# Kernel tuning notes

Measured on AMD Instinct MI355X. Metric: run time of the kernel, lower is better.

Reference implementation:

```python
import jax, jax.numpy as jnp
import numpy as np

B, S, H = 32, 8192, 512


def setup_inputs() -> dict:
    key = jax.random.key(0)
    k1, k2, k3, k4 = jax.random.split(key, 4)
    output = jax.random.normal(k1, (B, 1, H), dtype=jnp.float32)
    context = jax.random.normal(k2, (B, S, H), dtype=jnp.float32)
    split_index = jax.random.randint(k3, (B,), 1, S - 1)  # avoid all-masked softmax rows
    W = jax.random.normal(k4, (H, 4 * H), dtype=jnp.float32) * (1.0 / np.sqrt(4 * H))
    b = jnp.zeros((H,), dtype=jnp.float32)
    return {"output": output, "context": context, "split_index": split_index, "W": W, "b": b}


def reference(output, context, split_index, W, b):
    Bb, Ss, Hh = context.shape
    rows = jnp.arange(Bb)
    pos = jnp.arange(Ss)

    # attn = bmm(output, context^T).squeeze(1) -> [B, S]
    attn = jnp.einsum('bih,bsh->bis', output, context)[:, 0, :]
    # torch code uses attn.data (detached) for all softmax paths
    attn_d = jax.lax.stop_gradient(attn)

    # forward-side mask: positions i < split_index kept
    fmask = pos[None, :] < split_index[:, None]  # [B, S] bool
    f_logits = jnp.where(fmask, attn_d, -jnp.inf)
    f_attn = jax.nn.softmax(f_logits, axis=1)
    f_attn = f_attn.at[rows, split_index].set(0.0)  # explicit zero at split position
    a_mix = jnp.einsum('bs,bsh->bh', f_attn, context)[:, None, :]  # [B,1,H]

    # NOTE: original source has `b_attn = f_attn.view(...)` (bug), so b_mix == a_mix.
    # The b-side masked softmax is computed but dead; we replicate the realized math.
    b_mix = a_mix

    # det_att = context[b, split_index[b], :]
    det_att = context[rows, split_index][:, None, :]  # [B,1,H]

    combined = jnp.concatenate((a_mix, b_mix, det_att, output), axis=2)  # [B,1,4H]
    out = jnp.tanh(combined @ W.T + b)  # Linear(4H->H) + Tanh, [B,1,H]
    return out, attn
```

## Files before the change

### kernel.cpp

```cpp
#include <hip/hip_runtime.h>
#include <math.h>

#define BATCH 32
#define SEQ   8192
#define HID   512
#define STRIPES 16
#define RPB   (SEQ / STRIPES)
#define CR    16
#define NCHUNK (RPB / CR)

typedef float f4 __attribute__((ext_vector_type(4)));

#define VMWAIT(N) do { asm volatile("s_waitcnt vmcnt(" #N ")" ::: "memory"); \
                       __builtin_amdgcn_sched_barrier(0); } while (0)
#define LGKMWAIT0 do { asm volatile("s_waitcnt lgkmcnt(0)" ::: "memory"); \
                       __builtin_amdgcn_sched_barrier(0); } while (0)

__device__ __forceinline__ void gload_lds(const float* g, float* l) {
  __builtin_amdgcn_global_load_lds(
      (const __attribute__((address_space(1))) void*)g,
      (__attribute__((address_space(3))) void*)l, 16, 0, 0);
}

__global__ __launch_bounds__(256, 2) void k_pass1(
    const float* __restrict__ outp, const float* __restrict__ ctx,
    const int* __restrict__ split, float* __restrict__ attn_out,
    float* __restrict__ pacc, float* __restrict__ pmd)
{
  __shared__ float lds[2][CR][HID];
  const int tid = threadIdx.x, lane = tid & 63, wave = tid >> 6;
  const int b = blockIdx.x >> 4;
  const int stripe = blockIdx.x & 15;
  const int sp = split[b];
  const int s_base = stripe * RPB;

  const float* ob = outp + b * HID + lane * 8;
  const f4 o0 = *(const f4*)ob;
  const f4 o1 = *(const f4*)(ob + 4);

  const float* cbase = ctx + ((size_t)b * SEQ + s_base) * HID;
  float* ao = attn_out + (size_t)b * SEQ + s_base;

#pragma unroll
  for (int i = 0; i < 8; ++i) {
    const int o = (wave * 8 + i) * 256;
    gload_lds(cbase + o + lane * 4, &lds[0][0][0] + o);
  }
#pragma unroll
  for (int i = 0; i < 8; ++i) {
    const int o = (wave * 8 + i) * 256;
    gload_lds(cbase + CR * HID + o + lane * 4, &lds[1][0][0] + o);
  }

  float m = -INFINITY, d = 0.f;
  f4 acc0 = {0.f, 0.f, 0.f, 0.f}, acc1 = {0.f, 0.f, 0.f, 0.f};

#pragma unroll 1
  for (int c = 0; c < NCHUNK; ++c) {
    if (c == 0)                 VMWAIT(8);
    else if (c == NCHUNK - 1)   VMWAIT(1);
    else                        VMWAIT(9);

    const int cur = c & 1;
    f4 c0[4], c1[4];
#pragma unroll
    for (int k = 0; k < 4; ++k) {
      const float* rp = &lds[cur][wave * 4 + k][lane * 8];
      c0[k] = *(const f4*)rp;
      c1[k] = *(const f4*)(rp + 4);
    }
    LGKMWAIT0;

    if (c + 2 < NCHUNK) {
      const float* src = cbase + (size_t)(c + 2) * CR * HID;
      float* dst = &lds[cur][0][0];
#pragma unroll
      for (int i = 0; i < 8; ++i) {
        const int o = (wave * 8 + i) * 256;
        gload_lds(src + o + lane * 4, dst + o);
      }
    }

    float a4[4];
#pragma unroll
    for (int k = 0; k < 4; ++k) {
      float v = o0[0]*c0[k][0] + o0[1]*c0[k][1] + o0[2]*c0[k][2] + o0[3]*c0[k][3]
              + o1[0]*c1[k][0] + o1[1]*c1[k][1] + o1[2]*c1[k][2] + o1[3]*c1[k][3];
#pragma unroll
      for (int off = 32; off >= 1; off >>= 1) v += __shfl_xor(v, off, 64);
      a4[k] = v;
    }
    if (lane == 0) {
      f4 st = {a4[0], a4[1], a4[2], a4[3]};
      *(f4*)(ao + c * CR + wave * 4) = st;
    }
#pragma unroll
    for (int k = 0; k < 4; ++k) {
      const int s = s_base + c * CR + wave * 4 + k;
      if (s < sp) {
        const float v  = a4[k];
        const float nm = fmaxf(m, v);
        const float sc = __expf(m - nm);
        const float w  = __expf(v - nm);
        d = d * sc + w;
        acc0 = acc0 * sc + w * c0[k];
        acc1 = acc1 * sc + w * c1[k];
        m = nm;
      }
    }
  }

  __syncthreads();
  float* lacc = &lds[0][0][0];
  float* lmd  = &lds[1][0][0];
  *(f4*)(lacc + wave * HID + lane * 8)     = acc0;
  *(f4*)(lacc + wave * HID + lane * 8 + 4) = acc1;
  if (lane == 0) { lmd[wave * 2] = m; lmd[wave * 2 + 1] = d; }
  __syncthreads();

  const float M = fmaxf(fmaxf(lmd[0], lmd[2]), fmaxf(lmd[4], lmd[6]));
  const size_t pb = (size_t)b * STRIPES + stripe;
  float* pa = pacc + pb * HID;
  if (M == -INFINITY) {
    pa[tid * 2] = 0.f; pa[tid * 2 + 1] = 0.f;
    if (tid == 0) { pmd[pb * 2] = -INFINITY; pmd[pb * 2 + 1] = 0.f; }
  } else {
    float e[4], Dl = 0.f;
#pragma unroll
    for (int wv = 0; wv < 4; ++wv) {
      const float mw = lmd[wv * 2];
      e[wv] = (mw == -INFINITY) ? 0.f : __expf(mw - M);
      Dl += e[wv] * lmd[wv * 2 + 1];
    }
    float s0 = 0.f, s1 = 0.f;
#pragma unroll
    for (int wv = 0; wv < 4; ++wv) {
      s0 += e[wv] * lacc[wv * HID + tid * 2];
      s1 += e[wv] * lacc[wv * HID + tid * 2 + 1];
    }
    pa[tid * 2] = s0; pa[tid * 2 + 1] = s1;
    if (tid == 0) { pmd[pb * 2] = M; pmd[pb * 2 + 1] = Dl; }
  }
}

__global__ __launch_bounds__(256) void k_final(
    const float* __restrict__ outp, const float* __restrict__ ctx,
    const int* __restrict__ split, const float* __restrict__ W,
    const float* __restrict__ bias, const float* __restrict__ pacc,
    const float* __restrict__ pmd, float* __restrict__ out0)
{
  const int b = blockIdx.x >> 3, q = blockIdx.x & 7;
  const int tid = threadIdx.x;
  __shared__ float comb[3 * HID + 8];
  float* amixp = comb;
  float* detp  = comb + HID + 4;
  float* oupp  = comb + 2 * HID + 8;

  float M = -INFINITY;
#pragma unroll
  for (int c = 0; c < STRIPES; ++c) M = fmaxf(M, pmd[(b * STRIPES + c) * 2]);
  float wgt[STRIPES], D = 0.f;
#pragma unroll
  for (int c = 0; c < STRIPES; ++c) {
    const float mw = pmd[(b * STRIPES + c) * 2];
    wgt[c] = (mw == -INFINITY) ? 0.f : __expf(mw - M);
    D += wgt[c] * pmd[(b * STRIPES + c) * 2 + 1];
  }
  const float invD = 1.f / D;
  const int sp = split[b];
#pragma unroll
  for (int col = tid; col < HID; col += 256) {
    float s = 0.f;
#pragma unroll
    for (int c = 0; c < STRIPES; ++c)
      s += wgt[c] * pacc[((size_t)(b * STRIPES + c)) * HID + col];
    amixp[col] = s * invD;
    detp[col]  = ctx[((size_t)b * SEQ + sp) * HID + col];
    oupp[col]  = outp[b * HID + col];
  }
  __syncthreads();

  const int hl = tid >> 2, part = tid & 3;
  const int h = q * 64 + hl;
  const float* wr = W + (size_t)h * (4 * HID) + part * HID;
  const float* src = (part == 2) ? detp : (part == 3 ? oupp : amixp);
  float acc = 0.f;
#pragma unroll 4
  for (int k0 = 0; k0 < HID; k0 += 4) {
    const f4 w = *(const f4*)(wr + k0);
    const f4 x = *(const f4*)(src + k0);
    acc += w[0]*x[0] + w[1]*x[1] + w[2]*x[2] + w[3]*x[3];
  }
  acc += __shfl_xor(acc, 1, 64);
  acc += __shfl_xor(acc, 2, 64);
  if (part == 0) out0[b * HID + h] = tanhf(acc + bias[h]);
}

extern "C" void kernel_launch(void* const* d_in, const int* in_sizes, int n_in,
                              void* d_out, int out_size, void* d_ws, size_t ws_size,
                              hipStream_t stream)
{
  const float* outp = (const float*)d_in[0];
  const float* ctx  = (const float*)d_in[1];
  const int*   spl  = (const int*)d_in[2];
  const float* W    = (const float*)d_in[3];
  const float* bias = (const float*)d_in[4];

  float* out0   = (float*)d_out;
  float* attn_o = out0 + (size_t)BATCH * HID;

  float* pacc = (float*)d_ws;
  float* pmd  = pacc + (size_t)BATCH * STRIPES * HID;

  k_pass1<<<BATCH * STRIPES, 256, 0, stream>>>(outp, ctx, spl, attn_o, pacc, pmd);
  k_final<<<BATCH * 8,       256, 0, stream>>>(outp, ctx, spl, W, bias, pacc, pmd, out0);
}
```

Baseline: 122.9 us.

## Split final stage into combine and W-stationary GEMV, add nontemporal context loads

The final stage is split in two. A combine kernel writes the concatenated [a_mix, a_mix, det, output] vector per batch to workspace, and a GEMV kernel keeps each W row slice in registers while looping over all 32 batches. The old code re-read W once per batch, so this cuts W traffic by about 32x, at the cost of an extra kernel launch, a workspace round-trip, and only 64 blocks for the GEMV. Separately, the streaming context loads in pass 1 now use a nontemporal cache policy so they pollute the cache less.

```diff
diff --git a/kernel.cpp b/kernel.cpp
--- a/kernel.cpp
+++ b/kernel.cpp
@@ -10,16 +10,17 @@
 #define NCHUNK (RPB / CR)
 
 typedef float f4 __attribute__((ext_vector_type(4)));
+typedef float f2 __attribute__((ext_vector_type(2)));
 
 #define VMWAIT(N) do { asm volatile("s_waitcnt vmcnt(" #N ")" ::: "memory"); \
                        __builtin_amdgcn_sched_barrier(0); } while (0)
 #define LGKMWAIT0 do { asm volatile("s_waitcnt lgkmcnt(0)" ::: "memory"); \
                        __builtin_amdgcn_sched_barrier(0); } while (0)
 
-__device__ __forceinline__ void gload_lds(const float* g, float* l) {
+__device__ __forceinline__ void gload_lds_nt(const float* g, float* l) {
   __builtin_amdgcn_global_load_lds(
       (const __attribute__((address_space(1))) void*)g,
-      (__attribute__((address_space(3))) void*)l, 16, 0, 0);
+      (__attribute__((address_space(3))) void*)l, 16, 0, 2);
 }
 
 __global__ __launch_bounds__(256, 2) void k_pass1(
@@ -44,12 +45,12 @@
 #pragma unroll
   for (int i = 0; i < 8; ++i) {
     const int o = (wave * 8 + i) * 256;
-    gload_lds(cbase + o + lane * 4, &lds[0][0][0] + o);
+    gload_lds_nt(cbase + o + lane * 4, &lds[0][0][0] + o);
   }
 #pragma unroll
   for (int i = 0; i < 8; ++i) {
     const int o = (wave * 8 + i) * 256;
-    gload_lds(cbase + CR * HID + o + lane * 4, &lds[1][0][0] + o);
+    gload_lds_nt(cbase + CR * HID + o + lane * 4, &lds[1][0][0] + o);
   }
 
   float m = -INFINITY, d = 0.f;
@@ -77,7 +78,7 @@
 #pragma unroll
       for (int i = 0; i < 8; ++i) {
         const int o = (wave * 8 + i) * 256;
-        gload_lds(src + o + lane * 4, dst + o);
+        gload_lds_nt(src + o + lane * 4, dst + o);
       }
     }
 
@@ -143,19 +144,12 @@
   }
 }
 
-__global__ __launch_bounds__(256) void k_final(
+__global__ __launch_bounds__(256) void k_combine(
     const float* __restrict__ outp, const float* __restrict__ ctx,
-    const int* __restrict__ split, const float* __restrict__ W,
-    const float* __restrict__ bias, const float* __restrict__ pacc,
-    const float* __restrict__ pmd, float* __restrict__ out0)
-{
-  const int b = blockIdx.x >> 3, q = blockIdx.x & 7;
-  const int tid = threadIdx.x;
-  __shared__ float comb[3 * HID + 8];
-  float* amixp = comb;
-  float* detp  = comb + HID + 4;
-  float* oupp  = comb + 2 * HID + 8;
-
+    const int* __restrict__ split, const float* __restrict__ pacc,
+    const float* __restrict__ pmd, float* __restrict__ combined)
+{
+  const int b = blockIdx.x, tid = threadIdx.x;
   float M = -INFINITY;
 #pragma unroll
   for (int c = 0; c < STRIPES; ++c) M = fmaxf(M, pmd[(b * STRIPES + c) * 2]);
@@ -168,32 +162,48 @@
   }
   const float invD = 1.f / D;
   const int sp = split[b];
+  float* cb = combined + (size_t)b * (4 * HID);
 #pragma unroll
   for (int col = tid; col < HID; col += 256) {
     float s = 0.f;
 #pragma unroll
     for (int c = 0; c < STRIPES; ++c)
       s += wgt[c] * pacc[((size_t)(b * STRIPES + c)) * HID + col];
-    amixp[col] = s * invD;
-    detp[col]  = ctx[((size_t)b * SEQ + sp) * HID + col];
-    oupp[col]  = outp[b * HID + col];
-  }
-  __syncthreads();
-
-  const int hl = tid >> 2, part = tid & 3;
-  const int h = q * 64 + hl;
-  const float* wr = W + (size_t)h * (4 * HID) + part * HID;
-  const float* src = (part == 2) ? detp : (part == 3 ? oupp : amixp);
-  float acc = 0.f;
-#pragma unroll 4
-  for (int k0 = 0; k0 < HID; k0 += 4) {
-    const f4 w = *(const f4*)(wr + k0);
-    const f4 x = *(const f4*)(src + k0);
-    acc += w[0]*x[0] + w[1]*x[1] + w[2]*x[2] + w[3]*x[3];
-  }
-  acc += __shfl_xor(acc, 1, 64);
-  acc += __shfl_xor(acc, 2, 64);
-  if (part == 0) out0[b * HID + h] = tanhf(acc + bias[h]);
+    const float am = s * invD;
+    cb[col]           = am;
+    cb[HID + col]     = am;
+    cb[2 * HID + col] = ctx[((size_t)b * SEQ + sp) * HID + col];
+    cb[3 * HID + col] = outp[b * HID + col];
+  }
+}
+
+__global__ __launch_bounds__(256) void k_gemv(
+    const float* __restrict__ W, const float* __restrict__ bias,
+    const float* __restrict__ combined, float* __restrict__ out0)
+{
+  const int g = blockIdx.x;
+  const int r = threadIdx.x >> 5, t = threadIdx.x & 31;
+  const int h = g * 8 + r;
+
+  f4 wreg[16];
+  const float* wr = W + (size_t)h * (4 * HID) + t * 64;
+#pragma unroll
+  for (int i = 0; i < 16; ++i) wreg[i] = *(const f4*)(wr + i * 4);
+  const float bi = bias[h];
+
+#pragma unroll 1
+  for (int b = 0; b < BATCH; ++b) {
+    const float* cb = combined + (size_t)b * (4 * HID) + t * 64;
+    float acc = 0.f;
+#pragma unroll
+    for (int i = 0; i < 16; ++i) {
+      const f4 x = *(const f4*)(cb + i * 4);
+      acc += wreg[i][0]*x[0] + wreg[i][1]*x[1] + wreg[i][2]*x[2] + wreg[i][3]*x[3];
+    }
+#pragma unroll
+    for (int off = 16; off >= 1; off >>= 1) acc += __shfl_xor(acc, off, 64);
+    if (t == 0) out0[b * HID + h] = tanhf(acc + bi);
+  }
 }
 
 extern "C" void kernel_launch(void* const* d_in, const int* in_sizes, int n_in,
@@ -209,9 +219,11 @@
   float* out0   = (float*)d_out;
   float* attn_o = out0 + (size_t)BATCH * HID;
 
-  float* pacc = (float*)d_ws;
-  float* pmd  = pacc + (size_t)BATCH * STRIPES * HID;
-
-  k_pass1<<<BATCH * STRIPES, 256, 0, stream>>>(outp, ctx, spl, attn_o, pacc, pmd);
-  k_final<<<BATCH * 8,       256, 0, stream>>>(outp, ctx, spl, W, bias, pacc, pmd, out0);
-}
+  float* pacc     = (float*)d_ws;
+  float* pmd      = pacc + (size_t)BATCH * STRIPES * HID;
+  float* combined = pmd + (size_t)BATCH * STRIPES * 2;
+
+  k_pass1  <<<BATCH * STRIPES, 256, 0, stream>>>(outp, ctx, spl, attn_o, pacc, pmd);
+  k_combine<<<BATCH,           256, 0, stream>>>(outp, ctx, spl, pacc, pmd, combined);
+  k_gemv   <<<64,              256, 0, stream>>>(W, bias, combined, out0);
+}
```

Result: slower. 166.7 us (+35.7%).
